# Optimization experiments

Hardware: AMD Instinct MI355X
Metric: run time of the kernel (lower is better)

Reference implementation:

```python
import jax, jax.numpy as jnp
from jax import lax
import numpy as np

L, B, T, D_MODEL = 6, 8, 512, 2048
D_STATE, D_CONV, EXPAND = 128, 4, 2
D_INNER = EXPAND * D_MODEL
LN_EPS = 1e-5


def setup_inputs() -> dict:
    key = jax.random.key(0)
    ks = jax.random.split(key, 8)
    s = 0.02
    x = jax.random.normal(ks[0], (B, T, D_MODEL), jnp.float32)
    return {
        "x": x,
        "ln_g": jnp.ones((L, D_MODEL), jnp.float32),
        "ln_b": jnp.zeros((L, D_MODEL), jnp.float32),
        "W_in": jax.random.normal(ks[1], (L, 2 * D_INNER, D_MODEL), jnp.float32) * s,
        "conv_w": jax.random.normal(ks[2], (L, D_INNER, 1, D_CONV), jnp.float32) * s,
        "conv_b": jnp.zeros((L, D_INNER), jnp.float32),
        "W_xp": jax.random.normal(ks[3], (L, 2 * D_STATE, D_INNER), jnp.float32) * s,
        "W_dt": jax.random.normal(ks[4], (L, D_INNER, D_INNER), jnp.float32) * s,
        "b_dt": jnp.zeros((L, D_INNER), jnp.float32),
        "A_log": jnp.broadcast_to(jnp.log(jnp.arange(1, D_STATE + 1, dtype=jnp.float32)), (L, D_STATE)),
        "D_skip": jnp.ones((L, D_INNER), jnp.float32),
        "W_out": jax.random.normal(ks[5], (L, D_MODEL, D_INNER), jnp.float32) * s,
    }


def _layernorm(x, g, b):
    mu = x.mean(-1, keepdims=True)
    var = ((x - mu) ** 2).mean(-1, keepdims=True)
    return (x - mu) * lax.rsqrt(var + LN_EPS) * g + b


def _ssm(xc, W_xp, b_dt_W, A_log, D_skip):
    # xc: [B, T, D_INNER]
    W_xp_w, W_dt_w, b_dt = b_dt_W
    A = -jnp.exp(A_log)                                   # [S]
    bc = jnp.einsum('btd,sd->bts', xc, W_xp_w)            # [B,T,2S]
    B_state, C_state = jnp.split(bc, 2, axis=-1)          # [B,T,S] each
    delta = jax.nn.softplus(jnp.einsum('btd,ed->bte', xc, W_dt_w) + b_dt)
    delta_mean = delta.mean(-1)                           # [B,T] scalar dt per step
    A_disc = jnp.exp(delta_mean[..., None] * A)           # [B,T,S]

    def step(h, inp):
        a_t, b_t, c_t = inp                               # [B,S] each
        h = h * a_t + b_t
        return h, jnp.sum(h * c_t, axis=-1)               # carry, [B]

    init = jnp.zeros((xc.shape[0], A_log.shape[0]), xc.dtype)
    _, ys = lax.scan(step, init,
                     (A_disc.transpose(1, 0, 2), B_state.transpose(1, 0, 2), C_state.transpose(1, 0, 2)))
    y = ys.T[..., None]                                   # [B,T,1] broadcast over d_inner
    return y + D_skip * xc


def _mamba_block(x, ln_g, ln_b, W_in, conv_w, conv_b, W_xp, W_dt, b_dt, A_log, D_skip, W_out):
    x_n = _layernorm(x, ln_g, ln_b)
    x_and_res = jnp.einsum('btd,ed->bte', x_n, W_in)      # [B,T,2*D_INNER]
    x_p, res = jnp.split(x_and_res, 2, axis=-1)
    # causal depthwise conv1d: torch pads (d_conv-1) both sides then trims [:T]
    xc = lax.conv_general_dilated(x_p.transpose(0, 2, 1), conv_w,
                                  window_strides=(1,), padding=[(D_CONV - 1, 0)],
                                  feature_group_count=D_INNER,
                                  dimension_numbers=('NCH', 'OIH', 'NCH'))
    xc = (xc + conv_b[None, :, None]).transpose(0, 2, 1)  # [B,T,D_INNER]
    xc = jax.nn.silu(xc)
    y = _ssm(xc, W_xp, (W_xp, W_dt, b_dt), A_log, D_skip)
    y = y * jax.nn.silu(res)
    out = jnp.einsum('btd,md->btm', y, W_out)
    return out + x


def reference(x, ln_g, ln_b, W_in, conv_w, conv_b, W_xp, W_dt, b_dt, A_log, D_skip, W_out):
    h = x
    for i in range(L):
        h = _mamba_block(h, ln_g[i], ln_b[i], W_in[i], conv_w[i], conv_b[i],
                         W_xp[i], W_dt[i], b_dt[i], A_log[i], D_skip[i], W_out[i])
    return h
```

## Files before the change

### kernel.cpp

```cpp
#include <hip/hip_runtime.h>
#include <hip/hip_bf16.h>

#define NLAYERS 6
#define BB 8
#define TT 512
#define DMODEL 2048
#define DSTATE 128
#define DCONV 4
#define DINNER 4096
#define NTOK (BB*TT)
#define NKSPLIT_XP 16
#define NCVT 20992

typedef __bf16 bf16x8 __attribute__((ext_vector_type(8)));
typedef float floatx4 __attribute__((ext_vector_type(4)));
typedef unsigned short ushort8v __attribute__((ext_vector_type(8)));
typedef unsigned short ushort4v __attribute__((ext_vector_type(4)));

__device__ __forceinline__ float bf2f(unsigned short u) {
    return __uint_as_float(((unsigned)u) << 16);
}
__device__ __forceinline__ unsigned short f2bf(float f) {
    unsigned u = __float_as_uint(f);
    unsigned r = u + 0x7FFFu + ((u >> 16) & 1u);
    return (unsigned short)(r >> 16);
}
__device__ __forceinline__ float siluf(float x) { return x / (1.f + __expf(-x)); }
__device__ __forceinline__ float softplusf(float x) {
    return fmaxf(x, 0.f) + log1pf(__expf(-fabsf(x)));
}

__device__ __forceinline__ void gload16(const void* g, void* l) {
    __builtin_amdgcn_global_load_lds(
        (const __attribute__((address_space(1))) void*)g,
        (__attribute__((address_space(3))) void*)l, 16, 0, 0);
}

__device__ __forceinline__ int2 pack_fp8x8(const float* v, float scale) {
    int lo = __builtin_amdgcn_cvt_pk_fp8_f32(v[0] * scale, v[1] * scale, 0, false);
    lo = __builtin_amdgcn_cvt_pk_fp8_f32(v[2] * scale, v[3] * scale, lo, true);
    int hi = __builtin_amdgcn_cvt_pk_fp8_f32(v[4] * scale, v[5] * scale, 0, false);
    hi = __builtin_amdgcn_cvt_pk_fp8_f32(v[6] * scale, v[7] * scale, hi, true);
    int2 o = {lo, hi};
    return o;
}

#define BARR __builtin_amdgcn_s_barrier()
#define SCHB __builtin_amdgcn_sched_barrier(0)
#define PRIO1 __builtin_amdgcn_s_setprio(1)
#define PRIO0 __builtin_amdgcn_s_setprio(0)

__global__ __launch_bounds__(256) void cvtln_kernel(const float* __restrict__ Win,
                                                    const float* __restrict__ Wdt,
                                                    const float* __restrict__ Wxp,
                                                    const float* __restrict__ Wout,
                                                    unsigned char* __restrict__ dIn,
                                                    unsigned char* __restrict__ dDt,
                                                    unsigned char* __restrict__ dXp,
                                                    unsigned char* __restrict__ dOut,
                                                    float* __restrict__ dmean,
                                                    const float* __restrict__ p0,
                                                    const float* __restrict__ p1,
                                                    const float* __restrict__ hin,
                                                    const float* __restrict__ g,
                                                    const float* __restrict__ b,
                                                    int hasP,
                                                    float* __restrict__ hout,
                                                    unsigned char* __restrict__ out8) {
    if (blockIdx.x < NTOK) {
        const int row = blockIdx.x;
        const long rb = (long)row * DMODEL;
        const int base = threadIdx.x * 8;
        float vv[8];
        float4 v0 = *(const float4*)(hin + rb + base);
        float4 v1 = *(const float4*)(hin + rb + base + 4);
        vv[0]=v0.x; vv[1]=v0.y; vv[2]=v0.z; vv[3]=v0.w;
        vv[4]=v1.x; vv[5]=v1.y; vv[6]=v1.z; vv[7]=v1.w;
        if (hasP) {
            float4 a0 = *(const float4*)(p0 + rb + base);
            float4 a1 = *(const float4*)(p0 + rb + base + 4);
            float4 c0 = *(const float4*)(p1 + rb + base);
            float4 c1 = *(const float4*)(p1 + rb + base + 4);
            vv[0]+=a0.x+c0.x; vv[1]+=a0.y+c0.y; vv[2]+=a0.z+c0.z; vv[3]+=a0.w+c0.w;
            vv[4]+=a1.x+c1.x; vv[5]+=a1.y+c1.y; vv[6]+=a1.z+c1.z; vv[7]+=a1.w+c1.w;
            float4 w0 = {vv[0],vv[1],vv[2],vv[3]}, w1 = {vv[4],vv[5],vv[6],vv[7]};
            *(float4*)(hout + rb + base) = w0;
            *(float4*)(hout + rb + base + 4) = w1;
        }
        float s = 0.f, s2 = 0.f;
#pragma unroll
        for (int j = 0; j < 8; j++) { s += vv[j]; s2 += vv[j] * vv[j]; }
#pragma unroll
        for (int off = 32; off >= 1; off >>= 1) {
            s += __shfl_xor(s, off);
            s2 += __shfl_xor(s2, off);
        }
        __shared__ float red[8];
        int wave = threadIdx.x >> 6, lane = threadIdx.x & 63;
        if (lane == 0) { red[wave] = s; red[4 + wave] = s2; }
        __syncthreads();
        s = red[0] + red[1] + red[2] + red[3];
        s2 = red[4] + red[5] + red[6] + red[7];
        float mu = s * (1.f / DMODEL);
        float var = s2 * (1.f / DMODEL) - mu * mu;
        float rs = rsqrtf(var + 1e-5f);
        float nv[8];
#pragma unroll
        for (int j = 0; j < 8; j++)
            nv[j] = (vv[j] - mu) * rs * g[base + j] + b[base + j];
        *(int2*)&out8[rb + base] = pack_fp8x8(nv, 4.f);
    } else {
        const long nWin  = (long)2 * DINNER * DMODEL;
        const long nWdt  = (long)DINNER * DINNER;
        const long nWxp  = (long)2 * DSTATE * DINNER;
        const long cum1 = nWin, cum2 = cum1 + nWdt, cum3 = cum2 + nWxp;
        const int cb = blockIdx.x - NTOK;
        long i = (long)cb * 2048 + threadIdx.x * 8;
        const float* s; unsigned char* d; long off;
        if (i < cum1)      { s = Win;  d = dIn;  off = i; }
        else if (i < cum2) { s = Wdt;  d = dDt;  off = i - cum1; }
        else if (i < cum3) { s = Wxp;  d = dXp;  off = i - cum2; }
        else               { s = Wout; d = dOut; off = i - cum3; }
        float v[8];
        float4 v0 = *(const float4*)(s + off);
        float4 v1 = *(const float4*)(s + off + 4);
        v[0]=v0.x; v[1]=v0.y; v[2]=v0.z; v[3]=v0.w;
        v[4]=v1.x; v[5]=v1.y; v[6]=v1.z; v[7]=v1.w;
        *(int2*)(d + off) = pack_fp8x8(v, 64.f);
        if (cb < 8) {
            float2 z = {0.f, 0.f};
            *(float2*)&dmean[(cb * 256 + threadIdx.x) * 2] = z;
        }
    }
}

__global__ __launch_bounds__(256) void combine3_kernel(const float* __restrict__ p0,
                                                       const float* __restrict__ p1,
                                                       const float* __restrict__ h,
                                                       float* __restrict__ out) {
    long i = (long)(blockIdx.x * blockDim.x + threadIdx.x) * 4;
    float4 a = *(const float4*)(p0 + i);
    float4 b = *(const float4*)(p1 + i);
    float4 c = *(const float4*)(h + i);
    float4 o = {a.x+b.x+c.x, a.y+b.y+c.y, a.z+b.z+c.z, a.w+b.w+c.w};
    *(float4*)(out + i) = o;
}

template <int EPI>
__global__ __launch_bounds__(512, 1) void gemm8(const unsigned char* __restrict__ A8,
                                                const unsigned char* __restrict__ B8,
                                                const unsigned char* __restrict__ Bx8,
                                                int KstrB, int KT, int ldc,
                                                unsigned short* __restrict__ obf,
                                                float* __restrict__ of0,
                                                float* __restrict__ of1,
                                                const float* __restrict__ bias,
                                                float* __restrict__ dmean,
                                                float SC) {
    __shared__ __align__(16) char lds[5 * 32768];
    const int tid = threadIdx.x;
    const int w = tid >> 6, lane = tid & 63;
    const int wm = w >> 2, wn = w & 3;

    int by, bx = 0, kpart = 0, KTloc = KT;
    bool isXp = false;
    const unsigned char* Bsel = B8;
    if constexpr (EPI == 4) {
        isXp = blockIdx.x >= 256;
        const int b2 = isXp ? (blockIdx.x - 256) : blockIdx.x;
        const int xcd = b2 & 7;
        const int l = b2 >> 3;
        by = xcd * 2 + (l & 1);
        const int rest = l >> 1;
        if (isXp) { kpart = rest; KTloc = 4; Bsel = Bx8; }
        else { bx = rest; KTloc = 64; }
    } else {
        const int xcd = blockIdx.x & 7;
        const int l = blockIdx.x >> 3;
        by = xcd * 2 + (l & 1);
        const int rest = l >> 1;
        if constexpr (EPI == 3) { bx = rest & 7; kpart = rest >> 3; }
        else { bx = rest; }
    }
    const long rowBase = (long)by * 256;
    const long colBase = (long)bx * 256;
    const long K0b = (long)kpart * KTloc * 64;

    int cbs[2];
#pragma unroll
    for (int s = 0; s < 2; s++)
        cbs[s] = (((((lane & 1) << 2) | (s * 2 + (lane >> 5))) ^ ((lane >> 1) & 7)) * 16)
                 + ((lane >> 4) & 1) * 8;
    const char* rdA = lds + wm * 8192 + ((lane >> 1) & 7) * 128;
    const char* rdB = lds + 16384 + wn * 4096 + ((lane >> 1) & 7) * 128;

    const int t8 = tid >> 3;
    const int ch3 = (tid & 7) ^ (t8 & 7);
    const int srow = 2 * t8 + (ch3 >> 2);
    const int coff = (ch3 & 3) * 16;
    const size_t Kb = (size_t)KstrB;
    const char* pA1 = (const char*)A8 + (rowBase + srow) * Kb + coff + K0b;
    const char* pA2 = (const char*)A8 + (rowBase + 128 + srow) * Kb + coff + K0b;
    const char* pB1 = (const char*)Bsel + (colBase + srow) * Kb + coff + K0b;
    const char* pB2 = (const char*)Bsel + (colBase + 128 + srow) * Kb + coff + K0b;
    const long wb = (long)w * 1024;

    floatx4 acc[8][4];
#pragma unroll
    for (int m = 0; m < 8; m++)
#pragma unroll
        for (int n = 0; n < 4; n++) acc[m][n] = floatx4{0.f, 0.f, 0.f, 0.f};

#define STG8(BUF, OFF) do { \
    gload16(pA1 + (OFF), lds + (BUF)*32768 + wb); \
    gload16(pA2 + (OFF), lds + (BUF)*32768 + 8192 + wb); \
    gload16(pB1 + (OFF), lds + (BUF)*32768 + 16384 + wb); \
    gload16(pB2 + (OFF), lds + (BUF)*32768 + 24576 + wb); } while(0)

    STG8(0, 0);
    STG8(1, (size_t)((1 < KTloc) ? 1 : KTloc - 1) * 64);
    STG8(2, (size_t)((2 < KTloc) ? 2 : KTloc - 1) * 64);
    STG8(3, (size_t)((3 < KTloc) ? 3 : KTloc - 1) * 64);

    for (int t = 0; t < KTloc; t++) {
        const long bo = (long)(t % 5) * 32768;
        const int bufS = (t + 4) % 5;
        const size_t off4 = (size_t)((t + 4 < KTloc) ? (t + 4) : (KTloc - 1)) * 64;
        asm volatile("s_waitcnt vmcnt(12)");
        BARR;
        STG8(bufS, off4);
        long b0[4], a0[8], b1[4], a1[8];
#pragma unroll
        for (int n = 0; n < 4; n++) b0[n] = *(const long*)(rdB + bo + n * 1024 + cbs[0]);
#pragma unroll
        for (int m = 0; m < 8; m++) a0[m] = *(const long*)(rdA + bo + m * 1024 + cbs[0]);
#pragma unroll
        for (int n = 0; n < 4; n++) b1[n] = *(const long*)(rdB + bo + n * 1024 + cbs[1]);
#pragma unroll
        for (int m = 0; m < 8; m++) a1[m] = *(const long*)(rdA + bo + m * 1024 + cbs[1]);
        asm volatile("s_waitcnt lgkmcnt(12)"); SCHB;
        PRIO1;
#pragma unroll
        for (int m = 0; m < 8; m++)
#pragma unroll
            for (int n = 0; n < 4; n++)
                acc[m][n] = __builtin_amdgcn_mfma_f32_16x16x32_fp8_fp8(b0[n], a0[m], acc[m][n], 0, 0, 0);
        PRIO0;
        asm volatile("s_waitcnt lgkmcnt(0)"); SCHB;
        PRIO1;
#pragma unroll
        for (int m = 0; m < 8; m++)
#pragma unroll
            for (int n = 0; n < 4; n++)
                acc[m][n] = __builtin_amdgcn_mfma_f32_16x16x32_fp8_fp8(b1[n], a1[m], acc[m][n], 0, 0, 0);
        PRIO0;
    }
#undef STG8

    const int lrow = lane & 15, cg = (lane >> 4) * 4;
    if constexpr (EPI == 0) {
#pragma unroll
        for (int mi = 0; mi < 8; mi++)
#pragma unroll
            for (int n = 0; n < 4; n++) {
                long row = rowBase + wm * 128 + mi * 16 + lrow;
                long col = colBase + wn * 64 + n * 16 + cg;
                ushort4v o = {f2bf(acc[mi][n][0] * SC), f2bf(acc[mi][n][1] * SC),
                              f2bf(acc[mi][n][2] * SC), f2bf(acc[mi][n][3] * SC)};
                *(ushort4v*)&obf[row * ldc + col] = o;
            }
    } else if constexpr (EPI == 3) {
        float* op = (kpart == 0) ? of0 : of1;
#pragma unroll
        for (int mi = 0; mi < 8; mi++)
#pragma unroll
            for (int n = 0; n < 4; n++) {
                long row = rowBase + wm * 128 + mi * 16 + lrow;
                long col = colBase + wn * 64 + n * 16 + cg;
                *(floatx4*)&op[row * ldc + col] = acc[mi][n] * SC;
            }
    } else {
        if (!isXp) {
            float4 bi[4];
#pragma unroll
            for (int n = 0; n < 4; n++)
                bi[n] = *(const float4*)&bias[colBase + wn * 64 + n * 16 + cg];
#pragma unroll
            for (int mi = 0; mi < 8; mi++) {
                float s = 0.f;
#pragma unroll
                for (int n = 0; n < 4; n++) {
                    s += softplusf(acc[mi][n][0] * SC + bi[n].x);
                    s += softplusf(acc[mi][n][1] * SC + bi[n].y);
                    s += softplusf(acc[mi][n][2] * SC + bi[n].z);
                    s += softplusf(acc[mi][n][3] * SC + bi[n].w);
                }
                s += __shfl_xor(s, 16);
                s += __shfl_xor(s, 32);
                if ((lane >> 4) == 0)
                    atomicAdd(&dmean[rowBase + wm * 128 + mi * 16 + lrow], s);
            }
        } else {
            float* op = of0 + (long)kpart * NTOK * 256;
#pragma unroll
            for (int mi = 0; mi < 8; mi++)
#pragma unroll
                for (int n = 0; n < 4; n++) {
                    long row = rowBase + wm * 128 + mi * 16 + lrow;
                    long col = wn * 64 + n * 16 + cg;
                    *(floatx4*)&op[row * 256 + col] = acc[mi][n] * SC;
                }
        }
    }
}

__global__ __launch_bounds__(256) void conv_silu4_kernel(const unsigned short* __restrict__ xr,
                                                         const float* __restrict__ w,
                                                         const float* __restrict__ cb,
                                                         unsigned short* __restrict__ xc,
                                                         unsigned char* __restrict__ xc8) {
    int idx = blockIdx.x * 256 + threadIdx.x;
    int d0 = (idx & 511) * 8;
    int g = idx >> 9;
    int bt0 = g * 4;
    int t0 = bt0 & (TT - 1);
    float rows[7][8];
#pragma unroll
    for (int j = 0; j < 7; j++) {
        if (t0 - 3 + j < 0) {
#pragma unroll
            for (int e = 0; e < 8; e++) rows[j][e] = 0.f;
        } else {
            ushort8v v = *(const ushort8v*)&xr[(long)(bt0 - 3 + j) * (2 * DINNER) + d0];
#pragma unroll
            for (int e = 0; e < 8; e++) rows[j][e] = bf2f(v[e]);
        }
    }
    float4 wv[8];
#pragma unroll
    for (int e = 0; e < 8; e++) wv[e] = *(const float4*)&w[(d0 + e) * DCONV];
    float cbv[8];
#pragma unroll
    for (int e = 0; e < 8; e++) cbv[e] = cb[d0 + e];
#pragma unroll
    for (int tj = 0; tj < 4; tj++) {
        float sv[8];
        ushort8v ov;
#pragma unroll
        for (int e = 0; e < 8; e++) {
            float a = cbv[e];
            a += rows[tj][e] * wv[e].x;
            a += rows[tj + 1][e] * wv[e].y;
            a += rows[tj + 2][e] * wv[e].z;
            a += rows[tj + 3][e] * wv[e].w;
            sv[e] = siluf(a);
            ov[e] = f2bf(sv[e]);
        }
        *(ushort8v*)&xc[(long)(bt0 + tj) * DINNER + d0] = ov;
        *(int2*)&xc8[(long)(bt0 + tj) * DINNER + d0] = pack_fp8x8(sv, 4.f);
    }
}

__global__ __launch_bounds__(256) void bcsum_kernel(const float* __restrict__ bcp,
                                                    float* __restrict__ bc) {
    long i = (long)(blockIdx.x * blockDim.x + threadIdx.x) * 4;
    const long S = (long)NTOK * 256;
    float4 o = *(const float4*)(bcp + i);
#pragma unroll
    for (int p = 1; p < NKSPLIT_XP; p++) {
        float4 v = *(const float4*)(bcp + (long)p * S + i);
        o.x += v.x; o.y += v.y; o.z += v.z; o.w += v.w;
    }
    *(float4*)(bc + i) = o;
}

__global__ void scan_kernel(const float* __restrict__ dmean, const float* __restrict__ bcmat,
                            const float* __restrict__ A_log, float* __restrict__ ys) {
    int b = blockIdx.x, lane = threadIdx.x;
    float A0 = -expf(A_log[lane]);
    float A1 = -expf(A_log[lane + 64]);
    float h0 = 0.f, h1 = 0.f;
    const float inv = 1.f / (float)DINNER;
    const float* rowp = bcmat + (long)b * TT * (2 * DSTATE);
    const float* dmp = dmean + b * TT;

    float cB0[4], cB1[4], cC0[4], cC1[4]; float4 cDM;
    float nB0[4], nB1[4], nC0[4], nC1[4]; float4 nDM;

#define LOADB(B0_, B1_, C0_, C1_, DM_, T0) do { \
    int tt_ = (T0); if (tt_ > TT - 4) tt_ = TT - 4; \
    _Pragma("unroll") for (int j_ = 0; j_ < 4; j_++) { \
        const float* rp_ = rowp + (long)(tt_ + j_) * 256; \
        B0_[j_] = rp_[lane]; B1_[j_] = rp_[64 + lane]; \
        C0_[j_] = rp_[128 + lane]; C1_[j_] = rp_[192 + lane]; } \
    DM_ = *(const float4*)&dmp[tt_]; } while (0)

#define COMPUTE4(B0_, B1_, C0_, C1_, DM_, T0) do { \
    float vv_[4]; \
    const float dms_[4] = {DM_.x, DM_.y, DM_.z, DM_.w}; \
    _Pragma("unroll") for (int j_ = 0; j_ < 4; j_++) { \
        float dm_ = dms_[j_] * inv; \
        h0 = h0 * __expf(dm_ * A0) + B0_[j_]; \
        h1 = h1 * __expf(dm_ * A1) + B1_[j_]; \
        vv_[j_] = h0 * C0_[j_] + h1 * C1_[j_]; } \
    _Pragma("unroll") for (int off_ = 32; off_ >= 1; off_ >>= 1) { \
        vv_[0] += __shfl_xor(vv_[0], off_); vv_[1] += __shfl_xor(vv_[1], off_); \
        vv_[2] += __shfl_xor(vv_[2], off_); vv_[3] += __shfl_xor(vv_[3], off_); } \
    if (lane == 0) { \
        float4 o_ = {vv_[0], vv_[1], vv_[2], vv_[3]}; \
        *(float4*)&ys[b * TT + (T0)] = o_; } } while (0)

    LOADB(cB0, cB1, cC0, cC1, cDM, 0);
    LOADB(nB0, nB1, nC0, nC1, nDM, 4);

    for (int t0 = 0; t0 < TT; t0 += 8) {
        COMPUTE4(cB0, cB1, cC0, cC1, cDM, t0);
        LOADB(cB0, cB1, cC0, cC1, cDM, t0 + 8);
        COMPUTE4(nB0, nB1, nC0, nC1, nDM, t0 + 4);
        LOADB(nB0, nB1, nC0, nC1, nDM, t0 + 12);
    }
#undef LOADB
#undef COMPUTE4
}

__global__ __launch_bounds__(256) void ycomb_kernel(const float* __restrict__ ys,
                                                    const unsigned short* __restrict__ xc,
                                                    const unsigned short* __restrict__ xr,
                                                    const float* __restrict__ dskip,
                                                    unsigned char* __restrict__ yc8) {
    int idx = blockIdx.x * blockDim.x + threadIdx.x;
    int d0 = (idx & 511) * 8;
    int bt = idx >> 9;
    float y = ys[bt];
    ushort8v xcv = *(const ushort8v*)&xc[(long)bt * DINNER + d0];
    ushort8v rv = *(const ushort8v*)&xr[(long)bt * (2 * DINNER) + DINNER + d0];
    float val[8];
#pragma unroll
    for (int j = 0; j < 8; j++)
        val[j] = (y + dskip[d0 + j] * bf2f(xcv[j])) * siluf(bf2f(rv[j]));
    *(int2*)&yc8[(long)bt * DINNER + d0] = pack_fp8x8(val, 16.f);
}

extern "C" void kernel_launch(void* const* d_in, const int* in_sizes, int n_in,
                              void* d_out, int out_size, void* d_ws, size_t ws_size,
                              hipStream_t stream) {
    const float* x      = (const float*)d_in[0];
    const float* ln_g   = (const float*)d_in[1];
    const float* ln_b   = (const float*)d_in[2];
    const float* W_in   = (const float*)d_in[3];
    const float* conv_w = (const float*)d_in[4];
    const float* conv_b = (const float*)d_in[5];
    const float* W_xp   = (const float*)d_in[6];
    const float* W_dt   = (const float*)d_in[7];
    const float* b_dt   = (const float*)d_in[8];
    const float* A_log  = (const float*)d_in[9];
    const float* D_skip = (const float*)d_in[10];
    const float* W_out  = (const float*)d_in[11];
    float* out = (float*)d_out;

    char* ws = (char*)d_ws;
    const size_t nWin  = (size_t)2 * DINNER * DMODEL;
    const size_t nWdt  = (size_t)DINNER * DINNER;
    const size_t nWxp  = (size_t)2 * DSTATE * DINNER;
    const size_t nWout = (size_t)DMODEL * DINNER;

    unsigned char* wb_in8  = (unsigned char*)ws; ws += nWin;
    unsigned char* wb_dt8  = (unsigned char*)ws; ws += nWdt;
    unsigned char* wb_xp8  = (unsigned char*)ws; ws += nWxp;
    unsigned char* wb_out8 = (unsigned char*)ws; ws += nWout;
    unsigned char* xn8 = (unsigned char*)ws; ws += (size_t)NTOK * DMODEL;
    unsigned short* xr = (unsigned short*)ws; ws += (size_t)NTOK * 2 * DINNER * 2;
    unsigned short* xc = (unsigned short*)ws; ws += (size_t)NTOK * DINNER * 2;
    unsigned char*  xc8 = (unsigned char*)ws; ws += (size_t)NTOK * DINNER;
    unsigned char*  yc8 = (unsigned char*)ws; ws += (size_t)NTOK * DINNER;
    float* bc    = (float*)ws; ws += (size_t)NTOK * 2 * DSTATE * 4;
    float* bcp   = (float*)ws; ws += (size_t)NKSPLIT_XP * NTOK * 2 * DSTATE * 4;
    float* dmean = (float*)ws; ws += (size_t)NTOK * 4;
    float* ysb   = (float*)ws; ws += (size_t)NTOK * 4;
    float* h0    = (float*)ws; ws += (size_t)NTOK * DMODEL * 4;
    float* h1    = (float*)ws; ws += (size_t)NTOK * DMODEL * 4;
    float* p0    = (float*)ws; ws += (size_t)NTOK * DMODEL * 4;
    float* p1    = (float*)ws; ws += (size_t)NTOK * DMODEL * 4;

    const float* hprev = x;
    for (int lay = 0; lay < NLAYERS; lay++) {
        float* hcur = (lay & 1) ? h1 : h0;
        cvtln_kernel<<<NTOK + NCVT, 256, 0, stream>>>(
            W_in + (size_t)lay * nWin, W_dt + (size_t)lay * nWdt,
            W_xp + (size_t)lay * nWxp, W_out + (size_t)lay * nWout,
            wb_in8, wb_dt8, wb_xp8, wb_out8, dmean,
            p0, p1, hprev, ln_g + lay * DMODEL, ln_b + lay * DMODEL,
            lay > 0 ? 1 : 0, hcur, xn8);
        if (lay > 0) hprev = hcur;

        gemm8<0><<<512, 512, 0, stream>>>(xn8, wb_in8, nullptr, DMODEL, 32, 2 * DINNER,
                                          xr, nullptr, nullptr, nullptr, nullptr, 1.f / 256.f);

        conv_silu4_kernel<<<NTOK / 4 * 512 / 256, 256, 0, stream>>>(
            xr, conv_w + (size_t)lay * DINNER * DCONV, conv_b + (size_t)lay * DINNER, xc, xc8);

        gemm8<4><<<512, 512, 0, stream>>>(xc8, wb_dt8, wb_xp8, DINNER, 64, 0,
                                          nullptr, bcp, nullptr,
                                          b_dt + (size_t)lay * DINNER, dmean, 1.f / 256.f);

        bcsum_kernel<<<(NTOK * 256 / 4) / 256, 256, 0, stream>>>(bcp, bc);

        scan_kernel<<<BB, 64, 0, stream>>>(dmean, bc, A_log + (size_t)lay * DSTATE, ysb);

        ycomb_kernel<<<NTOK * 512 / 256, 256, 0, stream>>>(
            ysb, xc, xr, D_skip + (size_t)lay * DINNER, yc8);

        gemm8<3><<<256, 512, 0, stream>>>(yc8, wb_out8, nullptr, DINNER, 32, DMODEL,
                                          nullptr, p0, p1, nullptr, nullptr, 1.f / 1024.f);
    }

    combine3_kernel<<<(NTOK * DMODEL / 4) / 256, 256, 0, stream>>>(p0, p1, hprev, out);

    (void)in_sizes; (void)n_in; (void)out_size; (void)ws_size;
}
```

Before: 3.112 ms.

## Replace in-proj GEMM with 128x256 tile kernel, fp8 residual, and halve xp k-split

Adds a dedicated in-projection GEMM using 128x256 tiles, 256 threads, two blocks per CU and a 3-stage LDS pipeline. It writes the conv input as bf16 and the gate (res) half directly as fp8. The bf16 xc buffer is dropped, so ycomb now reads fp8 xc8 and res8 instead of bf16, cutting intermediate memory traffic. The xp k-split is halved to 8, shrinking the partial-sum buffer and the bcsum work but giving each block a longer K loop. Reading xc and res from fp8 adds quantization error to the gating path.

```diff
diff --git a/kernel.cpp b/kernel.cpp
--- a/kernel.cpp
+++ b/kernel.cpp
@@ -9,7 +9,7 @@
 #define DCONV 4
 #define DINNER 4096
 #define NTOK (BB*TT)
-#define NKSPLIT_XP 16
+#define NKSPLIT_XP 8
 #define NCVT 20992
 
 typedef __bf16 bf16x8 __attribute__((ext_vector_type(8)));
@@ -43,6 +43,13 @@
     hi = __builtin_amdgcn_cvt_pk_fp8_f32(v[6] * scale, v[7] * scale, hi, true);
     int2 o = {lo, hi};
     return o;
+}
+
+__device__ __forceinline__ void unpack_fp8x4(int wrd, float* o) {
+    o[0] = __builtin_amdgcn_cvt_f32_fp8(wrd, 0);
+    o[1] = __builtin_amdgcn_cvt_f32_fp8(wrd, 1);
+    o[2] = __builtin_amdgcn_cvt_f32_fp8(wrd, 2);
+    o[3] = __builtin_amdgcn_cvt_f32_fp8(wrd, 3);
 }
 
 #define BARR __builtin_amdgcn_s_barrier()
@@ -146,12 +153,130 @@
     *(float4*)(out + i) = o;
 }
 
+__global__ __launch_bounds__(256, 2) void gemm_in2b(const unsigned char* __restrict__ A8,
+                                                    const unsigned char* __restrict__ B8,
+                                                    unsigned short* __restrict__ xrp,
+                                                    unsigned char* __restrict__ res8) {
+    __shared__ __align__(16) char lds[3 * 24576];
+    const int tid = threadIdx.x;
+    const int w = tid >> 6, lane = tid & 63;
+    const int wm = w >> 1, wn = w & 1;
+
+    const int xcd = blockIdx.x & 7;
+    const int l = blockIdx.x >> 3;
+    const int by = xcd * 4 + (l & 3);
+    const int bx = l >> 2;
+    const long rowBase = (long)by * 128;
+    const long colBase = (long)bx * 256;
+
+    int cbs[2];
+#pragma unroll
+    for (int s = 0; s < 2; s++)
+        cbs[s] = (((((lane & 1) << 2) | (s * 2 + (lane >> 5))) ^ ((lane >> 1) & 7)) * 16)
+                 + ((lane >> 4) & 1) * 8;
+    const char* rdA = lds + wm * 4096 + ((lane >> 1) & 7) * 128;
+    const char* rdB = lds + 8192 + wn * 8192 + ((lane >> 1) & 7) * 128;
+
+    const int t8 = tid >> 3;
+    const int ch3 = (tid & 7) ^ (t8 & 7);
+    const int srow = 2 * t8 + (ch3 >> 2);
+    const int coff = (ch3 & 3) * 16;
+    const size_t Kb = (size_t)DMODEL;
+    const char* pA1 = (const char*)A8 + (rowBase + srow) * Kb + coff;
+    const char* pA2 = (const char*)A8 + (rowBase + 64 + srow) * Kb + coff;
+    const char* pB1 = (const char*)B8 + (colBase + srow) * Kb + coff;
+    const char* pB2 = (const char*)B8 + (colBase + 64 + srow) * Kb + coff;
+    const char* pB3 = (const char*)B8 + (colBase + 128 + srow) * Kb + coff;
+    const char* pB4 = (const char*)B8 + (colBase + 192 + srow) * Kb + coff;
+    const long wb = (long)w * 1024;
+
+    floatx4 acc[4][8];
+#pragma unroll
+    for (int m = 0; m < 4; m++)
+#pragma unroll
+        for (int n = 0; n < 8; n++) acc[m][n] = floatx4{0.f, 0.f, 0.f, 0.f};
+
+#define STG2(BUF, OFF) do { \
+    gload16(pA1 + (OFF), lds + (BUF)*24576 + wb); \
+    gload16(pA2 + (OFF), lds + (BUF)*24576 + 4096 + wb); \
+    gload16(pB1 + (OFF), lds + (BUF)*24576 + 8192 + wb); \
+    gload16(pB2 + (OFF), lds + (BUF)*24576 + 12288 + wb); \
+    gload16(pB3 + (OFF), lds + (BUF)*24576 + 16384 + wb); \
+    gload16(pB4 + (OFF), lds + (BUF)*24576 + 20480 + wb); } while(0)
+
+    const int KT = DMODEL / 64;
+    STG2(0, 0);
+    STG2(1, 64);
+
+    for (int t = 0; t < KT; t++) {
+        const long bo = (long)(t % 3) * 24576;
+        const int bufS = (t + 2) % 3;
+        const size_t off2 = (size_t)((t + 2 < KT) ? (t + 2) : (KT - 1)) * 64;
+        asm volatile("s_waitcnt vmcnt(6)");
+        BARR;
+        STG2(bufS, off2);
+        long b0[8], a0[4], b1[8], a1[4];
+#pragma unroll
+        for (int n = 0; n < 8; n++) b0[n] = *(const long*)(rdB + bo + n * 1024 + cbs[0]);
+#pragma unroll
+        for (int m = 0; m < 4; m++) a0[m] = *(const long*)(rdA + bo + m * 1024 + cbs[0]);
+#pragma unroll
+        for (int n = 0; n < 8; n++) b1[n] = *(const long*)(rdB + bo + n * 1024 + cbs[1]);
+#pragma unroll
+        for (int m = 0; m < 4; m++) a1[m] = *(const long*)(rdA + bo + m * 1024 + cbs[1]);
+        asm volatile("s_waitcnt lgkmcnt(12)"); SCHB;
+        PRIO1;
+#pragma unroll
+        for (int m = 0; m < 4; m++)
+#pragma unroll
+            for (int n = 0; n < 8; n++)
+                acc[m][n] = __builtin_amdgcn_mfma_f32_16x16x32_fp8_fp8(b0[n], a0[m], acc[m][n], 0, 0, 0);
+        PRIO0;
+        asm volatile("s_waitcnt lgkmcnt(0)"); SCHB;
+        PRIO1;
+#pragma unroll
+        for (int m = 0; m < 4; m++)
+#pragma unroll
+            for (int n = 0; n < 8; n++)
+                acc[m][n] = __builtin_amdgcn_mfma_f32_16x16x32_fp8_fp8(b1[n], a1[m], acc[m][n], 0, 0, 0);
+        PRIO0;
+    }
+#undef STG2
+
+    const int lrow = lane & 15, cg = (lane >> 4) * 4;
+    const float SC = 1.f / 256.f;
+    if (colBase < DINNER) {
+#pragma unroll
+        for (int mi = 0; mi < 4; mi++)
+#pragma unroll
+            for (int n = 0; n < 8; n++) {
+                long row = rowBase + wm * 64 + mi * 16 + lrow;
+                long col = colBase + wn * 128 + n * 16 + cg;
+                ushort4v o = {f2bf(acc[mi][n][0] * SC), f2bf(acc[mi][n][1] * SC),
+                              f2bf(acc[mi][n][2] * SC), f2bf(acc[mi][n][3] * SC)};
+                *(ushort4v*)&xrp[row * DINNER + col] = o;
+            }
+    } else {
+#pragma unroll
+        for (int mi = 0; mi < 4; mi++)
+#pragma unroll
+            for (int n = 0; n < 8; n++) {
+                long row = rowBase + wm * 64 + mi * 16 + lrow;
+                long col = colBase - DINNER + wn * 128 + n * 16 + cg;
+                int pw = __builtin_amdgcn_cvt_pk_fp8_f32(acc[mi][n][0] * SC * 16.f,
+                                                         acc[mi][n][1] * SC * 16.f, 0, false);
+                pw = __builtin_amdgcn_cvt_pk_fp8_f32(acc[mi][n][2] * SC * 16.f,
+                                                     acc[mi][n][3] * SC * 16.f, pw, true);
+                *(int*)&res8[row * DINNER + col] = pw;
+            }
+    }
+}
+
 template <int EPI>
 __global__ __launch_bounds__(512, 1) void gemm8(const unsigned char* __restrict__ A8,
                                                 const unsigned char* __restrict__ B8,
                                                 const unsigned char* __restrict__ Bx8,
                                                 int KstrB, int KT, int ldc,
-                                                unsigned short* __restrict__ obf,
                                                 float* __restrict__ of0,
                                                 float* __restrict__ of1,
                                                 const float* __restrict__ bias,
@@ -172,15 +297,14 @@
         const int l = b2 >> 3;
         by = xcd * 2 + (l & 1);
         const int rest = l >> 1;
-        if (isXp) { kpart = rest; KTloc = 4; Bsel = Bx8; }
+        if (isXp) { kpart = rest; KTloc = 8; Bsel = Bx8; }
         else { bx = rest; KTloc = 64; }
     } else {
         const int xcd = blockIdx.x & 7;
         const int l = blockIdx.x >> 3;
         by = xcd * 2 + (l & 1);
         const int rest = l >> 1;
-        if constexpr (EPI == 3) { bx = rest & 7; kpart = rest >> 3; }
-        else { bx = rest; }
+        bx = rest & 7; kpart = rest >> 3;
     }
     const long rowBase = (long)by * 256;
     const long colBase = (long)bx * 256;
@@ -258,18 +382,7 @@
 #undef STG8
 
     const int lrow = lane & 15, cg = (lane >> 4) * 4;
-    if constexpr (EPI == 0) {
-#pragma unroll
-        for (int mi = 0; mi < 8; mi++)
-#pragma unroll
-            for (int n = 0; n < 4; n++) {
-                long row = rowBase + wm * 128 + mi * 16 + lrow;
-                long col = colBase + wn * 64 + n * 16 + cg;
-                ushort4v o = {f2bf(acc[mi][n][0] * SC), f2bf(acc[mi][n][1] * SC),
-                              f2bf(acc[mi][n][2] * SC), f2bf(acc[mi][n][3] * SC)};
-                *(ushort4v*)&obf[row * ldc + col] = o;
-            }
-    } else if constexpr (EPI == 3) {
+    if constexpr (EPI == 3) {
         float* op = (kpart == 0) ? of0 : of1;
 #pragma unroll
         for (int mi = 0; mi < 8; mi++)
@@ -314,10 +427,9 @@
     }
 }
 
-__global__ __launch_bounds__(256) void conv_silu4_kernel(const unsigned short* __restrict__ xr,
+__global__ __launch_bounds__(256) void conv_silu4_kernel(const unsigned short* __restrict__ xrp,
                                                          const float* __restrict__ w,
                                                          const float* __restrict__ cb,
-                                                         unsigned short* __restrict__ xc,
                                                          unsigned char* __restrict__ xc8) {
     int idx = blockIdx.x * 256 + threadIdx.x;
     int d0 = (idx & 511) * 8;
@@ -331,7 +443,7 @@
 #pragma unroll
             for (int e = 0; e < 8; e++) rows[j][e] = 0.f;
         } else {
-            ushort8v v = *(const ushort8v*)&xr[(long)(bt0 - 3 + j) * (2 * DINNER) + d0];
+            ushort8v v = *(const ushort8v*)&xrp[(long)(bt0 - 3 + j) * DINNER + d0];
 #pragma unroll
             for (int e = 0; e < 8; e++) rows[j][e] = bf2f(v[e]);
         }
@@ -345,7 +457,6 @@
 #pragma unroll
     for (int tj = 0; tj < 4; tj++) {
         float sv[8];
-        ushort8v ov;
 #pragma unroll
         for (int e = 0; e < 8; e++) {
             float a = cbv[e];
@@ -354,9 +465,7 @@
             a += rows[tj + 2][e] * wv[e].z;
             a += rows[tj + 3][e] * wv[e].w;
             sv[e] = siluf(a);
-            ov[e] = f2bf(sv[e]);
         }
-        *(ushort8v*)&xc[(long)(bt0 + tj) * DINNER + d0] = ov;
         *(int2*)&xc8[(long)(bt0 + tj) * DINNER + d0] = pack_fp8x8(sv, 4.f);
     }
 }
@@ -424,20 +533,25 @@
 }
 
 __global__ __launch_bounds__(256) void ycomb_kernel(const float* __restrict__ ys,
-                                                    const unsigned short* __restrict__ xc,
-                                                    const unsigned short* __restrict__ xr,
+                                                    const unsigned char* __restrict__ xc8,
+                                                    const unsigned char* __restrict__ res8,
                                                     const float* __restrict__ dskip,
                                                     unsigned char* __restrict__ yc8) {
     int idx = blockIdx.x * blockDim.x + threadIdx.x;
     int d0 = (idx & 511) * 8;
     int bt = idx >> 9;
     float y = ys[bt];
-    ushort8v xcv = *(const ushort8v*)&xc[(long)bt * DINNER + d0];
-    ushort8v rv = *(const ushort8v*)&xr[(long)bt * (2 * DINNER) + DINNER + d0];
+    int2 xv = *(const int2*)&xc8[(long)bt * DINNER + d0];
+    int2 rv = *(const int2*)&res8[(long)bt * DINNER + d0];
+    float xf[8], rf[8];
+    unpack_fp8x4(xv.x, xf);
+    unpack_fp8x4(xv.y, xf + 4);
+    unpack_fp8x4(rv.x, rf);
+    unpack_fp8x4(rv.y, rf + 4);
     float val[8];
 #pragma unroll
     for (int j = 0; j < 8; j++)
-        val[j] = (y + dskip[d0 + j] * bf2f(xcv[j])) * siluf(bf2f(rv[j]));
+        val[j] = (y + dskip[d0 + j] * (xf[j] * 0.25f)) * siluf(rf[j] * 0.0625f);
     *(int2*)&yc8[(long)bt * DINNER + d0] = pack_fp8x8(val, 16.f);
 }
 
@@ -469,8 +583,8 @@
     unsigned char* wb_xp8  = (unsigned char*)ws; ws += nWxp;
     unsigned char* wb_out8 = (unsigned char*)ws; ws += nWout;
     unsigned char* xn8 = (unsigned char*)ws; ws += (size_t)NTOK * DMODEL;
-    unsigned short* xr = (unsigned short*)ws; ws += (size_t)NTOK * 2 * DINNER * 2;
-    unsigned short* xc = (unsigned short*)ws; ws += (size_t)NTOK * DINNER * 2;
+    unsigned short* xrp = (unsigned short*)ws; ws += (size_t)NTOK * DINNER * 2;
+    unsigned char*  res8 = (unsigned char*)ws; ws += (size_t)NTOK * DINNER;
     unsigned char*  xc8 = (unsigned char*)ws; ws += (size_t)NTOK * DINNER;
     unsigned char*  yc8 = (unsigned char*)ws; ws += (size_t)NTOK * DINNER;
     float* bc    = (float*)ws; ws += (size_t)NTOK * 2 * DSTATE * 4;
@@ -493,14 +607,13 @@
             lay > 0 ? 1 : 0, hcur, xn8);
         if (lay > 0) hprev = hcur;
 
-        gemm8<0><<<512, 512, 0, stream>>>(xn8, wb_in8, nullptr, DMODEL, 32, 2 * DINNER,
-                                          xr, nullptr, nullptr, nullptr, nullptr, 1.f / 256.f);
+        gemm_in2b<<<1024, 256, 0, stream>>>(xn8, wb_in8, xrp, res8);
 
         conv_silu4_kernel<<<NTOK / 4 * 512 / 256, 256, 0, stream>>>(
-            xr, conv_w + (size_t)lay * DINNER * DCONV, conv_b + (size_t)lay * DINNER, xc, xc8);
-
-        gemm8<4><<<512, 512, 0, stream>>>(xc8, wb_dt8, wb_xp8, DINNER, 64, 0,
-                                          nullptr, bcp, nullptr,
+            xrp, conv_w + (size_t)lay * DINNER * DCONV, conv_b + (size_t)lay * DINNER, xc8);
+
+        gemm8<4><<<384, 512, 0, stream>>>(xc8, wb_dt8, wb_xp8, DINNER, 64, 0,
+                                          bcp, nullptr,
                                           b_dt + (size_t)lay * DINNER, dmean, 1.f / 256.f);
 
         bcsum_kernel<<<(NTOK * 256 / 4) / 256, 256, 0, stream>>>(bcp, bc);
@@ -508,10 +621,10 @@
         scan_kernel<<<BB, 64, 0, stream>>>(dmean, bc, A_log + (size_t)lay * DSTATE, ysb);
 
         ycomb_kernel<<<NTOK * 512 / 256, 256, 0, stream>>>(
-            ysb, xc, xr, D_skip + (size_t)lay * DINNER, yc8);
+            ysb, xc8, res8, D_skip + (size_t)lay * DINNER, yc8);
 
         gemm8<3><<<256, 512, 0, stream>>>(yc8, wb_out8, nullptr, DINNER, 32, DMODEL,
-                                          nullptr, p0, p1, nullptr, nullptr, 1.f / 1024.f);
+                                          p0, p1, nullptr, nullptr, 1.f / 1024.f);
     }
 
     combine3_kernel<<<(NTOK * DMODEL / 4) / 256, 256, 0, stream>>>(p0, p1, hprev, out);
```

Measured after the change: 2.917 ms. -6.3%, faster.
